# Performance work log

Hardware: AMD Instinct MI355X
Metric: run time of the kernel (lower is better)

The kernel has to match this reference:

```python
import jax, jax.numpy as jnp
import numpy as np

IN_RES = 512.0        # model_input_resolution[0]
IOU_T = 0.75
SCORE_T = 0.25
MASK_T = 0.5
MAX_DET = 300         # fixed-size cap replacing dynamic NMS output


def setup_inputs() -> dict:
    key = jax.random.key(0)
    k1, k2, k3, k4, k5 = jax.random.split(key, 5)
    N = 5376  # anchors for 512x512 (64^2 + 32^2 + 16^2)
    cxcy = jax.random.uniform(k1, (1, 2, N)) * IN_RES
    wh = jax.random.uniform(k2, (1, 2, N)) * 120.0 + 8.0
    prob = jax.random.uniform(k3, (1, 4, N))          # 4 class scores
    coeff = jax.random.normal(k4, (1, 32, N)) * 0.5   # 32 mask coeffs
    boxes = jnp.concatenate([cxcy, wh, prob, coeff], axis=1)  # [1,40,N]
    proto = jax.random.normal(k5, (1, 128, 128, 32)) * 0.5
    return {"boxes": boxes, "proto": proto}


def _nms_fixed(boxes_yxyx, scores):
    """Greedy hard-NMS (same math as tf.raw_ops.NonMaxSuppressionV3) with a
    fixed MAX_DET output size; returns (orig indices, validity mask)."""
    N = scores.shape[0]
    order = jnp.argsort(-scores)
    bs = boxes_yxyx[order]
    ss = scores[order]
    y1, x1, y2, x2 = bs[:, 0], bs[:, 1], bs[:, 2], bs[:, 3]
    area = (y2 - y1) * (x2 - x1)
    iy1 = jnp.maximum(y1[:, None], y1[None, :])
    ix1 = jnp.maximum(x1[:, None], x1[None, :])
    iy2 = jnp.minimum(y2[:, None], y2[None, :])
    ix2 = jnp.minimum(x2[:, None], x2[None, :])
    inter = jnp.maximum(iy2 - iy1, 0.0) * jnp.maximum(ix2 - ix1, 0.0)
    iou = inter / (area[:, None] + area[None, :] - inter + 1e-9)  # [N,N]
    keep0 = ss >= SCORE_T
    idx = jnp.arange(N)
    def body(i, keep):
        sup = (iou[i] > IOU_T) & (idx > i)
        return jnp.where(keep[i], keep & ~sup, keep)
    keep = jax.lax.fori_loop(0, N, body, keep0)
    sel_sorted = jnp.nonzero(keep, size=MAX_DET, fill_value=N)[0]  # score-desc order
    valid = sel_sorted < N
    sel = order[jnp.clip(sel_sorted, 0, N - 1)]
    return sel, valid


def reference(boxes, proto):
    f32 = boxes.dtype
    b = boxes[0]                 # [40, N]
    prob = b[4:8]                # [4, N]
    coeff = b[8:]                # [32, N]
    box = b[:4]                  # [4, N] cx,cy,w,h
    p = proto[0]                 # [h, w, 32]

    cls = jnp.argmax(prob, axis=0)
    scores = jnp.max(prob, axis=0)

    bt = box.T                   # [N,4]
    xyxy = jnp.concatenate([bt[:, :2] - bt[:, 2:] / 2,
                            bt[:, :2] + bt[:, 2:] / 2], axis=-1)
    b_nms = xyxy[:, jnp.array([1, 0, 3, 2])]   # (y1,x1,y2,x2) for NMS

    sel, valid = _nms_fixed(b_nms, scores)
    vf = valid.astype(f32)

    boxes_sel = b_nms[sel] * vf[:, None]                     # [K,4]
    cls_sel = (cls[sel].astype(f32) * vf)[:, None]           # [K,1]
    scores_sel = (scores[sel] * vf)[:, None]                 # [K,1]
    coeff_sel = coeff[:, sel]                                # [32,K]

    # proto*coeff multiply-reduce-sigmoid (fused as einsum)
    m = jax.nn.sigmoid(jnp.einsum('hwc,ck->hwk', p, coeff_sel))  # [h,w,K]
    m = jnp.where(m >= MASK_T, m, jnp.zeros_like(m))
    m = m * vf[None, None, :]    # zero masks of padded (invalid) detections

    h, w, _ = m.shape
    ratio = jnp.asarray(IN_RES / h, dtype=f32)
    bb = boxes_sel / ratio
    # note: names follow original code; x1b is actually the row (y) min
    x1b, y1b, x2b, y2b = bb[:, 0], bb[:, 1], bb[:, 2], bb[:, 3]
    rows = jnp.arange(h, dtype=f32)[:, None, None]           # [h,1,1]
    cols = jnp.arange(w, dtype=f32)[None, :, None]           # [1,w,1]
    rmask = ((x1b <= rows) & (rows <= x2b)).astype(f32)       # [h,1,K]
    cmask = ((y1b <= cols) & (cols <= y2b)).astype(f32)       # [1,w,K]
    masks = jnp.sum(m * rmask * cmask, axis=-1)               # [h,w]

    return scores_sel, cls_sel, boxes_sel, masks
```

## Files before the change

### kernel.cpp

```cpp
#include <hip/hip_runtime.h>

#define N_BOX 5376
#define NQ4   1344
#define NCAND 1024
#define MAXD  300
#define NTH   1024
#define NBLK  129
#define NPRE  320
#define NPREB 5
#define RANK_TGT 768
#define FLOOR_B 2000
#define SCORE_T 0.25f

#define HSZ   4160
#define HSLOT(b) ((b) + ((b) >> 6))

#define MAGIC1 0x13579BDFu
#define MAGIC2 0x2468ACE1u

#define WS_DONE  0
#define WS_RRCC  16
#define WS_SEL   4816

typedef unsigned long long u64;
typedef unsigned int u32;
typedef unsigned short u16;

__device__ __forceinline__ int bucket_of(u32 u) {
    if (u >= 0x3F800000u) return 4095;
    return (u < 0x3F000000u) ? (int)(u >> 19) : 2016 + (int)((u - 0x3F000000u) >> 12);
}

__device__ __forceinline__ u32 cloadA(const u32* p) {
    return __hip_atomic_load(p, __ATOMIC_ACQUIRE, __HIP_MEMORY_SCOPE_AGENT);
}
__device__ __forceinline__ u32 cload32(const u32* p) {
    return __hip_atomic_load(p, __ATOMIC_RELAXED, __HIP_MEMORY_SCOPE_AGENT);
}
__device__ __forceinline__ u64 cload64(const u64* p) {
    return __hip_atomic_load(p, __ATOMIC_RELAXED, __HIP_MEMORY_SCOPE_AGENT);
}

union SMem {
    struct {
        int hist[HSZ];
        u16 basecopy[4096];
        u64 keys[NCAND];
        float4 cbox[NCAND];
        float4 selbox[MAXD];
        float4 batchb[64];
        u32 svals[N_BOX];
        u32 sclsp[NQ4];
        float4 scbox[NPRE];
        float sarea[NPRE];
        u64 supr[NPREB][NPRE];
        u64 selw[NPREB];
    } n;
    struct {
        float sco[MAXD * 32];
        float2 rl_c[MAXD];
        int rl_k[MAXD];
        float4 rc_all[MAXD];
        int sel_all[MAXD];
    } m;
};

__global__ __launch_bounds__(NTH) void k_fused(
        const float* __restrict__ boxes, const float* __restrict__ proto,
        float* __restrict__ out, char* __restrict__ ws)
{
    __shared__ SMem sm;
    __shared__ int thrvar, ncvar, scnt_s, rcount;

    const int bid = blockIdx.x, tid = threadIdx.x;

    u32*    done    = (u32*)(ws + WS_DONE);
    float4* ws_rrcc = (float4*)(ws + WS_RRCC);
    int*    ws_sel  = (int*)(ws + WS_SEL);

    if (bid >= 1) {
        const int r = bid - 1;
        const float rf = (float)r;

        float pr[32];
        if (tid < 128) {
            const float4* q = (const float4*)(proto + (((size_t)(r << 7) + tid) << 5));
            #pragma unroll
            for (int j = 0; j < 8; ++j) {
                float4 v = q[j];
                pr[4 * j + 0] = v.x; pr[4 * j + 1] = v.y;
                pr[4 * j + 2] = v.z; pr[4 * j + 3] = v.w;
            }
        }

        if (tid == 0) {
            for (;;) {
                if (cloadA(done) == MAGIC1 && cloadA(done + 1) == MAGIC2) break;
                __builtin_amdgcn_s_sleep(4);
            }
        }
        __syncthreads();

        if (tid < 600) {
            ((u64*)sm.m.rc_all)[tid] = cload64((const u64*)ws_rrcc + tid);
        } else if (tid >= 640 && tid < 640 + MAXD) {
            sm.m.sel_all[tid - 640] = (int)cload32((const u32*)ws_sel + (tid - 640));
        }
        __syncthreads();

        if (tid < 64) {
            int base = 0;
            for (int strip = 0; strip < 5; ++strip) {
                int k = strip * 64 + tid;
                bool flag = false; float4 rc = make_float4(1.f, 0.f, 1.f, 0.f);
                if (k < MAXD) {
                    rc = sm.m.rc_all[k];
                    flag = (rc.x <= rf) && (rf <= rc.y);
                }
                u64 m = __ballot(flag);
                int pos = base + (int)__popcll(m & ((1ull << tid) - 1ull));
                if (flag) { sm.m.rl_c[pos] = make_float2(rc.z, rc.w); sm.m.rl_k[pos] = k; }
                base += (int)__popcll(m);
            }
            if (tid == 0) rcount = base;
        }
        __syncthreads();
        const int L = rcount;

        for (int t = tid; t < L * 32; t += NTH) {
            int e = t >> 5, j = t & 31;
            int n = sm.m.sel_all[sm.m.rl_k[e]];
            n = (n < 0) ? 0 : n;
            sm.m.sco[t] = boxes[(8 + j) * N_BOX + n];
        }
        __syncthreads();

        if (tid < 128) {
            const float cf = (float)tid;
            float acc = 0.f;
            for (int e = 0; e < L; ++e) {
                float2 cc = sm.m.rl_c[e];
                if (cc.x <= cf && cf <= cc.y) {
                    const float* wv = &sm.m.sco[e << 5];
                    float d = 0.f;
                    #pragma unroll
                    for (int j = 0; j < 32; ++j) d = fmaf(pr[j], wv[j], d);
                    float sg = 1.f / (1.f + __expf(-d));
                    if (sg >= 0.5f) acc += sg;
                }
            }
            out[6 * MAXD + (r << 7) + tid] = acc;
        }
        return;
    }

    for (int b = tid; b < HSZ; b += NTH) sm.n.hist[b] = 0;
    for (int i = tid; i < NCAND; i += NTH) sm.n.keys[i] = 0;
    if (tid == 0) { thrvar = FLOOR_B; ncvar = 0; }
    __syncthreads();

    const float4* r0 = (const float4*)(boxes);
    const float4* r1 = (const float4*)(boxes + 1 * N_BOX);
    const float4* r2 = (const float4*)(boxes + 2 * N_BOX);
    const float4* r3 = (const float4*)(boxes + 3 * N_BOX);
    const float4* r4 = (const float4*)(boxes + 4 * N_BOX);
    const float4* r5 = (const float4*)(boxes + 5 * N_BOX);
    const float4* r6 = (const float4*)(boxes + 6 * N_BOX);
    const float4* r7 = (const float4*)(boxes + 7 * N_BOX);

    const int t0 = tid, t1 = tid + NTH;
    float4 xs0, ys0, ww0, hh0, xs1, ys1, ww1, hh1;

    auto p1_proc = [&](int t, float4& XS, float4& YS, float4& WV, float4& HS) {
        XS = r0[t]; YS = r1[t]; WV = r2[t]; HS = r3[t];
        float4 a = r4[t], b = r5[t], c = r6[t], d = r7[t];
        uint4 sv; u32 pk; float s; int cl;
        s = a.x; cl = 0;
        if (b.x > s) { s = b.x; cl = 1; }
        if (c.x > s) { s = c.x; cl = 2; }
        if (d.x > s) { s = d.x; cl = 3; }
        sv.x = __float_as_uint(s); pk = (u32)cl;
        s = a.y; cl = 0;
        if (b.y > s) { s = b.y; cl = 1; }
        if (c.y > s) { s = c.y; cl = 2; }
        if (d.y > s) { s = d.y; cl = 3; }
        sv.y = __float_as_uint(s); pk |= (u32)cl << 8;
        s = a.z; cl = 0;
        if (b.z > s) { s = b.z; cl = 1; }
        if (c.z > s) { s = c.z; cl = 2; }
        if (d.z > s) { s = d.z; cl = 3; }
        sv.z = __float_as_uint(s); pk |= (u32)cl << 16;
        s = a.w; cl = 0;
        if (b.w > s) { s = b.w; cl = 1; }
        if (c.w > s) { s = c.w; cl = 2; }
        if (d.w > s) { s = d.w; cl = 3; }
        sv.w = __float_as_uint(s); pk |= (u32)cl << 24;
        ((uint4*)sm.n.svals)[t] = sv;
        sm.n.sclsp[t] = pk;
        atomicAdd(&sm.n.hist[HSLOT(bucket_of(sv.x))], 1);
        atomicAdd(&sm.n.hist[HSLOT(bucket_of(sv.y))], 1);
        atomicAdd(&sm.n.hist[HSLOT(bucket_of(sv.z))], 1);
        atomicAdd(&sm.n.hist[HSLOT(bucket_of(sv.w))], 1);
    };
    p1_proc(t0, xs0, ys0, ww0, hh0);
    if (t1 < NQ4) p1_proc(t1, xs1, ys1, ww1, hh1);
    __syncthreads();

    if (tid < 64) {
        const int lane = tid;
        int csum = 0;
        for (int b = lane * 64; b < lane * 64 + 64; ++b) csum += sm.n.hist[HSLOT(b)];
        int incl = csum;
        for (int off = 1; off < 64; off <<= 1) {
            int t = __shfl_down(incl, off);
            if (lane + off < 64) incl += t;
        }
        int excl = __shfl_down(incl, 1);
        if (lane == 63) excl = 0;
        if (incl >= RANK_TGT && excl < RANK_TGT) {
            int cum = excl, thr = FLOOR_B;
            for (int b = lane * 64 + 63; b >= lane * 64; --b) {
                cum += sm.n.hist[HSLOT(b)];
                if (cum >= RANK_TGT) { thr = b; break; }
            }
            thrvar = (thr > FLOOR_B) ? thr : FLOOR_B;
        }
        int thr = thrvar;
        int run = excl;
        for (int b = lane * 64 + 63; b >= lane * 64; --b) {
            int h = sm.n.hist[HSLOT(b)];
            sm.n.hist[HSLOT(b)] = run;
            sm.n.basecopy[b] = (u16)run;
            if (b == thr) { int v = run + h; ncvar = (v < NCAND) ? v : NCAND; }
            run += h;
        }
    }
    __syncthreads();
    const int thr = thrvar;

    auto p4_scat = [&](int t, float4 xs, float4 ys, float4 wsv, float4 hs) {
        uint4 sv = ((const uint4*)sm.n.svals)[t];
        int b0 = bucket_of(sv.x), b1 = bucket_of(sv.y),
            b2 = bucket_of(sv.z), b3 = bucket_of(sv.w);
        int bm = max(max(b0, b1), max(b2, b3));
        if (bm < thr) return;
        u32 pk = sm.n.sclsp[t];
        int n = t << 2;
        if (b0 >= thr) {
            int pos = atomicAdd(&sm.n.hist[HSLOT(b0)], 1);
            if (pos < NCAND) {
                sm.n.cbox[pos] = make_float4(ys.x - 0.5f * hs.x, xs.x - 0.5f * wsv.x,
                                             ys.x + 0.5f * hs.x, xs.x + 0.5f * wsv.x);
                sm.n.keys[pos] = ((u64)sv.x << 25) | ((u64)(8191 - n) << 12)
                               | ((u64)(pk & 3u) << 10) | (u64)pos;
            }
        }
        if (b1 >= thr) {
            int pos = atomicAdd(&sm.n.hist[HSLOT(b1)], 1);
            if (pos < NCAND) {
                sm.n.cbox[pos] = make_float4(ys.y - 0.5f * hs.y, xs.y - 0.5f * wsv.y,
                                             ys.y + 0.5f * hs.y, xs.y + 0.5f * wsv.y);
                sm.n.keys[pos] = ((u64)sv.y << 25) | ((u64)(8191 - (n + 1)) << 12)
                               | ((u64)((pk >> 8) & 3u) << 10) | (u64)pos;
            }
        }
        if (b2 >= thr) {
            int pos = atomicAdd(&sm.n.hist[HSLOT(b2)], 1);
            if (pos < NCAND) {
                sm.n.cbox[pos] = make_float4(ys.z - 0.5f * hs.z, xs.z - 0.5f * wsv.z,
                                             ys.z + 0.5f * hs.z, xs.z + 0.5f * wsv.z);
                sm.n.keys[pos] = ((u64)sv.z << 25) | ((u64)(8191 - (n + 2)) << 12)
                               | ((u64)((pk >> 16) & 3u) << 10) | (u64)pos;
            }
        }
        if (b3 >= thr) {
            int pos = atomicAdd(&sm.n.hist[HSLOT(b3)], 1);
            if (pos < NCAND) {
                sm.n.cbox[pos] = make_float4(ys.w - 0.5f * hs.w, xs.w - 0.5f * wsv.w,
                                             ys.w + 0.5f * hs.w, xs.w + 0.5f * wsv.w);
                sm.n.keys[pos] = ((u64)sv.w << 25) | ((u64)(8191 - (n + 3)) << 12)
                               | ((u64)((pk >> 24) & 3u) << 10) | (u64)pos;
            }
        }
    };
    p4_scat(t0, xs0, ys0, ww0, hh0);
    if (t1 < NQ4) p4_scat(t1, xs1, ys1, ww1, hh1);
    __syncthreads();
    const int nc = ncvar;

    {
        u64 myk[2]; int mypos[2]; int cnt = 0;
        for (int p = tid; p < nc; p += NTH) {
            u64 kp = sm.n.keys[p];
            int b = bucket_of((u32)(kp >> 25));
            int start = (int)sm.n.basecopy[b];
            int end = sm.n.hist[HSLOT(b)]; if (end > NCAND) end = NCAND;
            int rank = 0;
            for (int q = start; q < end; ++q) rank += (sm.n.keys[q] > kp);
            myk[cnt] = kp; mypos[cnt] = start + rank; ++cnt;
        }
        __syncthreads();
        for (int i = 0; i < cnt; ++i) sm.n.keys[mypos[i]] = myk[i];
    }
    __syncthreads();

    {
        const int lim = (nc < NPRE) ? nc : NPRE;
        for (int c = tid; c < NPRE; c += NTH) {
            float4 bx = make_float4(0.f, 0.f, 0.f, 0.f);
            if (c < lim) bx = sm.n.cbox[(int)(sm.n.keys[c] & 0x3FFu)];
            sm.n.scbox[c] = bx;
            sm.n.sarea[c] = (bx.z - bx.x) * (bx.w - bx.y);
        }
    }
    for (int s = tid; s < MAXD; s += NTH) {
        ws_sel[s] = -1;
        ws_rrcc[s] = make_float4(1.f, 0.f, 1.f, 0.f);
    }
    __syncthreads();

    {
        const int wav = tid >> 6, lane = tid & 63;
        for (int t = wav; t < 15; t += NTH / 64) {
            int w, cb;
            if (t < 5)       { w = 0; cb = t << 6; }
            else if (t < 9)  { w = 1; cb = (t - 4) << 6; }
            else if (t < 12) { w = 2; cb = (t - 7) << 6; }
            else if (t < 14) { w = 3; cb = (t - 9) << 6; }
            else             { w = 4; cb = 256; }
            float4 qb = sm.n.scbox[(w << 6) + lane];
            float qa = sm.n.sarea[(w << 6) + lane];
            for (int c = cb; c < cb + 64; ++c) {
                float4 bx = sm.n.scbox[c];
                float ar = sm.n.sarea[c];
                float iy1 = fmaxf(bx.x, qb.x), ix1 = fmaxf(bx.y, qb.y);
                float iy2 = fminf(bx.z, qb.z), ix2 = fminf(bx.w, qb.w);
                float inter = fmaxf(iy2 - iy1, 0.f) * fmaxf(ix2 - ix1, 0.f);
                bool h = (1.75f * inter > 0.75f * (ar + qa) + 7.5e-10f);
                u64 m = __ballot(h);
                if (lane == 0) sm.n.supr[w][c] = m;
            }
        }
    }
    __syncthreads();

    if (tid < 64) {
        const int lane = tid;
        const u64 laneb = 1ull << lane;
        int scount = 0;
        for (int base = 0; base < nc; base += 64) {
            const int bidx = base >> 6;
            const bool pre = (base + 64 <= NPRE);
            int idx = base + lane;
            u64 k = 0;
            if (idx < nc) k = sm.n.keys[idx];
            float sc = __uint_as_float((u32)(k >> 25));
            bool valid = (idx < nc) && (sc >= SCORE_T);
            float4 bx = make_float4(0.f, 0.f, 0.f, 0.f);
            bool dead = false;
            u64 M = 0;
            if (pre) {
                if (valid) bx = sm.n.scbox[idx];
                #pragma unroll
                for (int w = 0; w < NPREB; ++w)
                    if (w < bidx)
                        dead = dead || ((sm.n.supr[w][idx] & sm.n.selw[w]) != 0ull);
                M = sm.n.supr[bidx][idx] & (laneb - 1ull);
            } else {
                if (valid) bx = sm.n.cbox[(int)(k & 0x3FFu)];
                sm.n.batchb[lane] = bx;
                float ar = (bx.z - bx.x) * (bx.w - bx.y);
                #pragma unroll 4
                for (int j = 0; j < scount; ++j) {
                    float4 sb = sm.n.selbox[j];
                    float sar = (sb.z - sb.x) * (sb.w - sb.y);
                    float iy1 = fmaxf(bx.x, sb.x), ix1 = fmaxf(bx.y, sb.y);
                    float iy2 = fminf(bx.z, sb.z), ix2 = fminf(bx.w, sb.w);
                    float inter = fmaxf(iy2 - iy1, 0.f) * fmaxf(ix2 - ix1, 0.f);
                    dead = dead || (1.75f * inter > 0.75f * (ar + sar) + 7.5e-10f);
                }
                #pragma unroll 4
                for (int q = 0; q < 64; ++q) {
                    float4 sb = sm.n.batchb[q];
                    float sar = (sb.z - sb.x) * (sb.w - sb.y);
                    float iy1 = fmaxf(bx.x, sb.x), ix1 = fmaxf(bx.y, sb.y);
                    float iy2 = fminf(bx.z, sb.z), ix2 = fminf(bx.w, sb.w);
                    float inter = fmaxf(iy2 - iy1, 0.f) * fmaxf(ix2 - ix1, 0.f);
                    bool h = (1.75f * inter > 0.75f * (ar + sar) + 7.5e-10f) && (q < lane);
                    if (h) M |= (1ull << q);
                }
            }

            u64 vmask  = __ballot(valid);
            u64 deadm  = __ballot(dead);
            u64 alive0 = vmask & ~deadm;
            u64 sel    = alive0;
            u64 conf   = __ballot((M & alive0) != 0ull) & alive0;
            while (conf) {
                int f = (int)__ffsll((unsigned long long)conf) - 1;
                conf &= conf - 1ull;
                u64 Mf = ((u64)(u32)__shfl((int)(M >> 32), f) << 32)
                       | (u64)(u32)__shfl((int)(M & 0xFFFFFFFFull), f);
                if (Mf & sel) sel &= ~(1ull << f);
            }
            if (pre && lane == 0) sm.n.selw[bidx] = sel;

            int navail = MAXD - scount;
            int myrank = (int)__popcll(sel & (laneb - 1ull));
            bool chosen = ((sel & laneb) != 0ull) && (myrank < navail);
            if (chosen) {
                int slot = scount + myrank;
                sm.n.selbox[slot] = bx;
                out[slot]        = sc;
                out[MAXD + slot] = (float)((k >> 10) & 3u);
                ((float4*)(out + 2 * MAXD))[slot] = bx;
                ws_sel[slot] = 8191 - (int)((k >> 12) & 0x1FFFu);
                ws_rrcc[slot] = make_float4(0.25f * bx.x, 0.25f * bx.z,
                                            0.25f * bx.y, 0.25f * bx.w);
            }
            int nsel = (int)__popcll(sel);
            if (nsel > navail) nsel = navail;
            scount += nsel;
            if (scount >= MAXD) break;
            if (vmask != 0xFFFFFFFFFFFFFFFFull) break;
        }
        if (lane == 0) scnt_s = scount;
    }
    __syncthreads();

    __threadfence();
    if (tid == 0) {
        __hip_atomic_store(done + 1, MAGIC2, __ATOMIC_RELEASE, __HIP_MEMORY_SCOPE_AGENT);
        __hip_atomic_store(done, MAGIC1, __ATOMIC_RELEASE, __HIP_MEMORY_SCOPE_AGENT);
    }

    const int c0f = scnt_s;
    for (int s = c0f + tid; s < MAXD; s += NTH) {
        out[s] = 0.f; out[MAXD + s] = 0.f;
        ((float4*)(out + 2 * MAXD))[s] = make_float4(0.f, 0.f, 0.f, 0.f);
    }
}

extern "C" void kernel_launch(void* const* d_in, const int* in_sizes, int n_in,
                              void* d_out, int out_size, void* d_ws, size_t ws_size,
                              hipStream_t stream) {
    const float* boxes = (const float*)d_in[0];
    const float* proto = (const float*)d_in[1];
    float* out = (float*)d_out;
    char* w = (char*)d_ws;

    hipLaunchKernelGGL(k_fused, dim3(NBLK), dim3(NTH), 0, stream,
                       boxes, proto, out, w);
}
```

Baseline: 32.30 us.

## Offload score/class/box preprocessing to 16 helper blocks via global workspace

Moves the per-anchor max-score, class argmax and box corner computation out of the single NMS block into 16 of the mask blocks, which write the results to a global workspace and signal readiness with release-store flags. Block 0 spins on the flags, then reads the precomputed scores, classes and boxes instead of loading all eight input rows itself. The goal is to shorten the serial front of block 0, at the cost of an extra global round trip, flag polling latency, and a dependency on the helper blocks being scheduled concurrently.

```diff
diff --git a/kernel.cpp b/kernel.cpp
--- a/kernel.cpp
+++ b/kernel.cpp
@@ -6,6 +6,8 @@
 #define MAXD  300
 #define NTH   1024
 #define NBLK  129
+#define NPREP 16
+#define PGRP  84
 #define NPRE  320
 #define NPREB 5
 #define RANK_TGT 768
@@ -19,8 +21,12 @@
 #define MAGIC2 0x2468ACE1u
 
 #define WS_DONE  0
-#define WS_RRCC  16
-#define WS_SEL   4816
+#define WS_PFLG  16
+#define WS_RRCC  144
+#define WS_SEL   4944
+#define WS_SVAL  6144
+#define WS_CLS   27648
+#define WS_CBOX  33024
 
 typedef unsigned long long u64;
 typedef unsigned int u32;
@@ -75,10 +81,73 @@
     const int bid = blockIdx.x, tid = threadIdx.x;
 
     u32*    done    = (u32*)(ws + WS_DONE);
+    u32*    pflg    = (u32*)(ws + WS_PFLG);
     float4* ws_rrcc = (float4*)(ws + WS_RRCC);
     int*    ws_sel  = (int*)(ws + WS_SEL);
+    u32*    ws_sval = (u32*)(ws + WS_SVAL);
+    u32*    ws_cls  = (u32*)(ws + WS_CLS);
+    float4* ws_cbox = (float4*)(ws + WS_CBOX);
 
     if (bid >= 1) {
+        if (bid <= NPREP) {
+            const int p = bid - 1;
+            if (tid < PGRP) {
+                const int t = p * PGRP + tid;
+                const float4* r0 = (const float4*)(boxes);
+                const float4* r1 = (const float4*)(boxes + 1 * N_BOX);
+                const float4* r2 = (const float4*)(boxes + 2 * N_BOX);
+                const float4* r3 = (const float4*)(boxes + 3 * N_BOX);
+                const float4* r4 = (const float4*)(boxes + 4 * N_BOX);
+                const float4* r5 = (const float4*)(boxes + 5 * N_BOX);
+                const float4* r6 = (const float4*)(boxes + 6 * N_BOX);
+                const float4* r7 = (const float4*)(boxes + 7 * N_BOX);
+
+                float4 a = r4[t], b = r5[t], c = r6[t], d = r7[t];
+                uint4 sv; u32 pk; float s; int cl;
+                s = a.x; cl = 0;
+                if (b.x > s) { s = b.x; cl = 1; }
+                if (c.x > s) { s = c.x; cl = 2; }
+                if (d.x > s) { s = d.x; cl = 3; }
+                sv.x = __float_as_uint(s); pk = (u32)cl;
+                s = a.y; cl = 0;
+                if (b.y > s) { s = b.y; cl = 1; }
+                if (c.y > s) { s = c.y; cl = 2; }
+                if (d.y > s) { s = d.y; cl = 3; }
+                sv.y = __float_as_uint(s); pk |= (u32)cl << 8;
+                s = a.z; cl = 0;
+                if (b.z > s) { s = b.z; cl = 1; }
+                if (c.z > s) { s = c.z; cl = 2; }
+                if (d.z > s) { s = d.z; cl = 3; }
+                sv.z = __float_as_uint(s); pk |= (u32)cl << 16;
+                s = a.w; cl = 0;
+                if (b.w > s) { s = b.w; cl = 1; }
+                if (c.w > s) { s = c.w; cl = 2; }
+                if (d.w > s) { s = d.w; cl = 3; }
+                sv.w = __float_as_uint(s); pk |= (u32)cl << 24;
+                ((uint4*)ws_sval)[t] = sv;
+                ws_cls[t] = pk;
+
+                float4 xs = r0[t], ys = r1[t], wv = r2[t], hs = r3[t];
+                int n = t << 2;
+                ws_cbox[n + 0] = make_float4(ys.x - 0.5f * hs.x, xs.x - 0.5f * wv.x,
+                                             ys.x + 0.5f * hs.x, xs.x + 0.5f * wv.x);
+                ws_cbox[n + 1] = make_float4(ys.y - 0.5f * hs.y, xs.y - 0.5f * wv.y,
+                                             ys.y + 0.5f * hs.y, xs.y + 0.5f * wv.y);
+                ws_cbox[n + 2] = make_float4(ys.z - 0.5f * hs.z, xs.z - 0.5f * wv.z,
+                                             ys.z + 0.5f * hs.z, xs.z + 0.5f * wv.z);
+                ws_cbox[n + 3] = make_float4(ys.w - 0.5f * hs.w, xs.w - 0.5f * wv.w,
+                                             ys.w + 0.5f * hs.w, xs.w + 0.5f * wv.w);
+            }
+            __syncthreads();
+            __threadfence();
+            if (tid == 0) {
+                __hip_atomic_store(&pflg[2 * p + 1], MAGIC2 - (u32)p,
+                                   __ATOMIC_RELEASE, __HIP_MEMORY_SCOPE_AGENT);
+                __hip_atomic_store(&pflg[2 * p], MAGIC1 + (u32)p,
+                                   __ATOMIC_RELEASE, __HIP_MEMORY_SCOPE_AGENT);
+            }
+        }
+
         const int r = bid - 1;
         const float rf = (float)r;
 
@@ -159,51 +228,25 @@
     if (tid == 0) { thrvar = FLOOR_B; ncvar = 0; }
     __syncthreads();
 
-    const float4* r0 = (const float4*)(boxes);
-    const float4* r1 = (const float4*)(boxes + 1 * N_BOX);
-    const float4* r2 = (const float4*)(boxes + 2 * N_BOX);
-    const float4* r3 = (const float4*)(boxes + 3 * N_BOX);
-    const float4* r4 = (const float4*)(boxes + 4 * N_BOX);
-    const float4* r5 = (const float4*)(boxes + 5 * N_BOX);
-    const float4* r6 = (const float4*)(boxes + 6 * N_BOX);
-    const float4* r7 = (const float4*)(boxes + 7 * N_BOX);
-
-    const int t0 = tid, t1 = tid + NTH;
-    float4 xs0, ys0, ww0, hh0, xs1, ys1, ww1, hh1;
-
-    auto p1_proc = [&](int t, float4& XS, float4& YS, float4& WV, float4& HS) {
-        XS = r0[t]; YS = r1[t]; WV = r2[t]; HS = r3[t];
-        float4 a = r4[t], b = r5[t], c = r6[t], d = r7[t];
-        uint4 sv; u32 pk; float s; int cl;
-        s = a.x; cl = 0;
-        if (b.x > s) { s = b.x; cl = 1; }
-        if (c.x > s) { s = c.x; cl = 2; }
-        if (d.x > s) { s = d.x; cl = 3; }
-        sv.x = __float_as_uint(s); pk = (u32)cl;
-        s = a.y; cl = 0;
-        if (b.y > s) { s = b.y; cl = 1; }
-        if (c.y > s) { s = c.y; cl = 2; }
-        if (d.y > s) { s = d.y; cl = 3; }
-        sv.y = __float_as_uint(s); pk |= (u32)cl << 8;
-        s = a.z; cl = 0;
-        if (b.z > s) { s = b.z; cl = 1; }
-        if (c.z > s) { s = c.z; cl = 2; }
-        if (d.z > s) { s = d.z; cl = 3; }
-        sv.z = __float_as_uint(s); pk |= (u32)cl << 16;
-        s = a.w; cl = 0;
-        if (b.w > s) { s = b.w; cl = 1; }
-        if (c.w > s) { s = c.w; cl = 2; }
-        if (d.w > s) { s = d.w; cl = 3; }
-        sv.w = __float_as_uint(s); pk |= (u32)cl << 24;
+    if (tid < NPREP) {
+        for (;;) {
+            if (cloadA(&pflg[2 * tid]) == MAGIC1 + (u32)tid &&
+                cloadA(&pflg[2 * tid + 1]) == MAGIC2 - (u32)tid) break;
+            __builtin_amdgcn_s_sleep(1);
+        }
+    }
+    __syncthreads();
+    __threadfence();
+
+    for (int t = tid; t < NQ4; t += NTH) {
+        uint4 sv = ((const uint4*)ws_sval)[t];
         ((uint4*)sm.n.svals)[t] = sv;
-        sm.n.sclsp[t] = pk;
+        sm.n.sclsp[t] = ws_cls[t];
         atomicAdd(&sm.n.hist[HSLOT(bucket_of(sv.x))], 1);
         atomicAdd(&sm.n.hist[HSLOT(bucket_of(sv.y))], 1);
         atomicAdd(&sm.n.hist[HSLOT(bucket_of(sv.z))], 1);
         atomicAdd(&sm.n.hist[HSLOT(bucket_of(sv.w))], 1);
-    };
-    p1_proc(t0, xs0, ys0, ww0, hh0);
-    if (t1 < NQ4) p1_proc(t1, xs1, ys1, ww1, hh1);
+    }
     __syncthreads();
 
     if (tid < 64) {
@@ -238,19 +281,18 @@
     __syncthreads();
     const int thr = thrvar;
 
-    auto p4_scat = [&](int t, float4 xs, float4 ys, float4 wsv, float4 hs) {
+    for (int t = tid; t < NQ4; t += NTH) {
         uint4 sv = ((const uint4*)sm.n.svals)[t];
         int b0 = bucket_of(sv.x), b1 = bucket_of(sv.y),
             b2 = bucket_of(sv.z), b3 = bucket_of(sv.w);
         int bm = max(max(b0, b1), max(b2, b3));
-        if (bm < thr) return;
+        if (bm < thr) continue;
         u32 pk = sm.n.sclsp[t];
         int n = t << 2;
         if (b0 >= thr) {
             int pos = atomicAdd(&sm.n.hist[HSLOT(b0)], 1);
             if (pos < NCAND) {
-                sm.n.cbox[pos] = make_float4(ys.x - 0.5f * hs.x, xs.x - 0.5f * wsv.x,
-                                             ys.x + 0.5f * hs.x, xs.x + 0.5f * wsv.x);
+                sm.n.cbox[pos] = ws_cbox[n + 0];
                 sm.n.keys[pos] = ((u64)sv.x << 25) | ((u64)(8191 - n) << 12)
                                | ((u64)(pk & 3u) << 10) | (u64)pos;
             }
@@ -258,8 +300,7 @@
         if (b1 >= thr) {
             int pos = atomicAdd(&sm.n.hist[HSLOT(b1)], 1);
             if (pos < NCAND) {
-                sm.n.cbox[pos] = make_float4(ys.y - 0.5f * hs.y, xs.y - 0.5f * wsv.y,
-                                             ys.y + 0.5f * hs.y, xs.y + 0.5f * wsv.y);
+                sm.n.cbox[pos] = ws_cbox[n + 1];
                 sm.n.keys[pos] = ((u64)sv.y << 25) | ((u64)(8191 - (n + 1)) << 12)
                                | ((u64)((pk >> 8) & 3u) << 10) | (u64)pos;
             }
@@ -267,8 +308,7 @@
         if (b2 >= thr) {
             int pos = atomicAdd(&sm.n.hist[HSLOT(b2)], 1);
             if (pos < NCAND) {
-                sm.n.cbox[pos] = make_float4(ys.z - 0.5f * hs.z, xs.z - 0.5f * wsv.z,
-                                             ys.z + 0.5f * hs.z, xs.z + 0.5f * wsv.z);
+                sm.n.cbox[pos] = ws_cbox[n + 2];
                 sm.n.keys[pos] = ((u64)sv.z << 25) | ((u64)(8191 - (n + 2)) << 12)
                                | ((u64)((pk >> 16) & 3u) << 10) | (u64)pos;
             }
@@ -276,15 +316,12 @@
         if (b3 >= thr) {
             int pos = atomicAdd(&sm.n.hist[HSLOT(b3)], 1);
             if (pos < NCAND) {
-                sm.n.cbox[pos] = make_float4(ys.w - 0.5f * hs.w, xs.w - 0.5f * wsv.w,
-                                             ys.w + 0.5f * hs.w, xs.w + 0.5f * wsv.w);
+                sm.n.cbox[pos] = ws_cbox[n + 3];
                 sm.n.keys[pos] = ((u64)sv.w << 25) | ((u64)(8191 - (n + 3)) << 12)
                                | ((u64)((pk >> 24) & 3u) << 10) | (u64)pos;
             }
         }
-    };
-    p4_scat(t0, xs0, ys0, ww0, hh0);
-    if (t1 < NQ4) p4_scat(t1, xs1, ys1, ww1, hh1);
+    }
     __syncthreads();
     const int nc = ncvar;
 
```

After: 40.87 us. +26.5%, slower.
